# Kernel optimization log

Hardware: AMD Instinct MI355X
Metric: run time of the kernel (lower is better)

Reference implementation:

```python
import jax, jax.numpy as jnp
import numpy as np

N_NODES = 100000
N_EDGES = 1000000
D_IN = 64
D_OUT = 64


def setup_inputs() -> dict:
    key = jax.random.key(0)
    k1, k2, k3, k4, k5 = jax.random.split(key, 5)
    x = jax.random.normal(k1, (N_NODES, D_IN), dtype=jnp.float32)
    W = jax.random.normal(k2, (D_OUT, D_IN), dtype=jnp.float32) / np.sqrt(D_IN)
    edge_weights = jax.random.uniform(k3, (N_EDGES,), dtype=jnp.float32)
    source = jax.random.randint(k4, (N_EDGES,), 0, N_NODES, dtype=jnp.int64 if jax.config.read('jax_enable_x64') else jnp.int32)
    target = jax.random.randint(k5, (N_EDGES,), 0, N_NODES, dtype=jnp.int64 if jax.config.read('jax_enable_x64') else jnp.int32)
    return {"x": x, "W": W, "edge_weights": edge_weights,
            "source": source, "target": target, "num_nodes": N_NODES}


def reference(x, W, edge_weights, source, target, num_nodes):
    # Linear (no bias): h = x @ W^T, shape (num_nodes, out)
    h = jnp.einsum('nd,od->no', x, W)
    # Gather messages per edge, scale by edge weights
    msg = h[source] * edge_weights[:, None]  # (num_edges, out)
    # Scatter-add by target node (sum aggregation)
    delta = jax.ops.segment_sum(msg, target, num_segments=num_nodes)
    return delta
```

## Files before the change

### kernel.cpp

```cpp
#include <hip/hip_runtime.h>


#define D     64
#define BKT   64
#define BSH   6
#define NBMAX 2048
#define CAP   1024

__global__ __launch_bounds__(256) void gcn_scatter_kernel(
    const float* __restrict__ x, const float* __restrict__ ew,
    const int* __restrict__ src, const int* __restrict__ tgt,
    float* __restrict__ s, int n_edges)
{
    int lane = threadIdx.x & 63;
    int e = blockIdx.x * 4 + (threadIdx.x >> 6);
    if (e >= n_edges) return;
    int sn = src[e];
    int tn = tgt[e];
    float w = ew[e];
    float v = x[(size_t)sn * D + lane] * w;
    atomicAdd(&s[(size_t)tn * D + lane], v);
}

__global__ __launch_bounds__(256) void gcn_gemm_kernel(
    const float* __restrict__ s, const float* __restrict__ W,
    float* __restrict__ out, int n_nodes)
{
    __shared__ float4 xs[64 * 17];
    const int tid  = threadIdx.x;
    const int lane = tid & 63;
    const int wid  = __builtin_amdgcn_readfirstlane(tid >> 6);
    const int row0 = blockIdx.x * 64;

    const float4* s4 = reinterpret_cast<const float4*>(s);
#pragma unroll
    for (int k = 0; k < 4; ++k) {
        int f  = tid + k * 256;
        int r  = f >> 4;
        int c4 = f & 15;
        float4 v = make_float4(0.f, 0.f, 0.f, 0.f);
        if (row0 + r < n_nodes)
            v = s4[(size_t)(row0 + r) * 16 + c4];
        xs[r * 17 + c4] = v;
    }
    __syncthreads();

    float acc[16];
#pragma unroll
    for (int j = 0; j < 16; ++j) acc[j] = 0.f;

    const int o0 = wid * 16;
    const float4* W4 = reinterpret_cast<const float4*>(W);
#pragma unroll
    for (int d4 = 0; d4 < 16; ++d4) {
        float4 xv = xs[lane * 17 + d4];
#pragma unroll
        for (int j = 0; j < 16; ++j) {
            float4 wv = W4[(size_t)(o0 + j) * 16 + d4];
            acc[j] += xv.x * wv.x + xv.y * wv.y + xv.z * wv.z + xv.w * wv.w;
        }
    }

    const int row = row0 + lane;
    if (row < n_nodes) {
        float4* out4 = reinterpret_cast<float4*>(out);
#pragma unroll
        for (int j4 = 0; j4 < 4; ++j4) {
            float4 v = make_float4(acc[j4 * 4 + 0], acc[j4 * 4 + 1],
                                   acc[j4 * 4 + 2], acc[j4 * 4 + 3]);
            out4[(size_t)row * 16 + wid * 4 + j4] = v;
        }
    }
}

__device__ __forceinline__ unsigned f2bf(float f) {
    unsigned u = __float_as_uint(f);
    return (u + 0x7FFFu + ((u >> 16) & 1u)) >> 16;
}

__global__ __launch_bounds__(256) void convert_bf16_kernel(
    const float* __restrict__ x, uint2* __restrict__ xb, int n4)
{
    const float4* x4 = reinterpret_cast<const float4*>(x);
    int i = blockIdx.x * 256 + threadIdx.x;
    const int stride = gridDim.x * 256;
    for (; i < n4; i += stride) {
        float4 v = x4[i];
        uint2 o;
        o.x = f2bf(v.x) | (f2bf(v.y) << 16);
        o.y = f2bf(v.z) | (f2bf(v.w) << 16);
        xb[i] = o;
    }
}

__global__ __launch_bounds__(256) void bucket_hist_kernel(
    const int* __restrict__ tgt, int* __restrict__ bcnt,
    int n_edges, int nb, int epb)
{
    __shared__ int h[NBMAX];
    const int tid = threadIdx.x;
    for (int i = tid; i < nb; i += 256) h[i] = 0;
    __syncthreads();
    const int e0 = blockIdx.x * epb;
    const int e1 = min(e0 + epb, n_edges);
    for (int e = e0 + tid; e < e1; e += 256)
        atomicAdd(&h[tgt[e] >> BSH], 1);
    __syncthreads();
    for (int b = tid; b < nb; b += 256) {
        int c = h[b];
        if (c) atomicAdd(&bcnt[b], c);
    }
}

__global__ __launch_bounds__(1024) void bucket_scan_kernel(
    const int* __restrict__ bcnt, int* __restrict__ bstarts,
    int* __restrict__ bcur, int nb)
{
    __shared__ int lds[1024];
    const int tid = threadIdx.x;
    const int i0 = 2 * tid, i1 = 2 * tid + 1;
    int v0 = (i0 < nb) ? bcnt[i0] : 0;
    int v1 = (i1 < nb) ? bcnt[i1] : 0;
    int tsum = v0 + v1;
    lds[tid] = tsum;
    __syncthreads();
    for (int off = 1; off < 1024; off <<= 1) {
        int a = (tid >= off) ? lds[tid - off] : 0;
        __syncthreads();
        lds[tid] += a;
        __syncthreads();
    }
    int pre = lds[tid] - tsum;
    if (i0 < nb) { bstarts[i0] = pre;      bcur[i0] = pre; }
    if (i1 < nb) { bstarts[i1] = pre + v0; bcur[i1] = pre + v0; }
}

__global__ __launch_bounds__(256) void bucket_scatter_kernel(
    const int* __restrict__ src, const int* __restrict__ tgt,
    const float* __restrict__ ew, int* __restrict__ bcur,
    int2* __restrict__ pairs, int n_edges, int nb, int epb)
{
    __shared__ int h[NBMAX];
    __shared__ int base[NBMAX];
    const int tid = threadIdx.x;
    for (int i = tid; i < nb; i += 256) h[i] = 0;
    __syncthreads();
    const int e0 = blockIdx.x * epb;
    const int e1 = min(e0 + epb, n_edges);

    for (int e = e0 + tid; e < e1; e += 256)
        atomicAdd(&h[tgt[e] >> BSH], 1);
    __syncthreads();

    for (int b = tid; b < nb; b += 256) {
        int c = h[b];
        base[b] = c ? atomicAdd(&bcur[b], c) : 0;
        h[b] = 0;
    }
    __syncthreads();

    for (int e = e0 + tid; e < e1; e += 256) {
        int t = tgt[e];
        int b = t >> BSH;
        int r = atomicAdd(&h[b], 1);
        pairs[base[b] + r] =
            make_int2(((t & (BKT - 1)) << 24) | src[e], __float_as_int(ew[e]));
    }
}

__global__ __launch_bounds__(512, 6) void bucket_sort_reduce_gemm_kernel(
    const uint2* __restrict__ xb, const float* __restrict__ W,
    const int* __restrict__ bstarts, const int2* __restrict__ pairs,
    float* __restrict__ out, int n_nodes, int n_edges, int nb)
{
    __shared__ float Wl[64 * 66];
    __shared__ int2  ep[CAP];
    __shared__ int   segIncl[BKT];
    __shared__ int   rankc[BKT];
    __shared__ float accRow[8][64];

    const int tid  = threadIdx.x;
    const int lane = tid & 63;
    const int wv   = tid >> 6;
    const int q4   = lane >> 4;
    const int m    = lane & 15;

    for (int i = tid; i < 64 * 64; i += 512)
        Wl[(i >> 6) * 66 + (i & 63)] = W[i];

    const int b   = blockIdx.x;
    const int beg = bstarts[b];
    const int end = (b + 1 < nb) ? bstarts[b + 1] : n_edges;

    float4 acc[8];
#pragma unroll
    for (int s = 0; s < 8; ++s) acc[s] = make_float4(0.f, 0.f, 0.f, 0.f);

    for (int cbeg = beg; cbeg < end; cbeg += CAP) {
        const int ccnt = min(CAP, end - cbeg);

        if (tid < BKT) segIncl[tid] = 0;
        __syncthreads();

        for (int i = tid; i < ccnt; i += 512) {
            unsigned px = (unsigned)pairs[cbeg + i].x;
            atomicAdd(&segIncl[px >> 24], 1);
        }
        __syncthreads();

        int myc = (tid < BKT) ? segIncl[tid] : 0;
        __syncthreads();
        for (int off = 1; off < BKT; off <<= 1) {
            int a = (tid < BKT && tid >= off) ? segIncl[tid - off] : 0;
            __syncthreads();
            if (tid < BKT) segIncl[tid] += a;
            __syncthreads();
        }
        if (tid < BKT) rankc[tid] = segIncl[tid] - myc;
        __syncthreads();

        for (int i = tid; i < ccnt; i += 512) {
            int2 p = pairs[cbeg + i];
            int tl = ((unsigned)p.x) >> 24;
            int pos = atomicAdd(&rankc[tl], 1);
            ep[pos] = p;
        }
        __syncthreads();

#pragma unroll
        for (int s = 0; s < 8; ++s) {
            const int tl = s * 8 + wv;
            const int s0 = __builtin_amdgcn_readfirstlane(tl ? segIncl[tl - 1] : 0);
            const int s1 = __builtin_amdgcn_readfirstlane(segIncl[tl]);
            float4 a = acc[s];
            for (int e = s0; e < s1; e += 8) {
                const int ea = e + q4;
                const int eb = e + 4 + q4;
                int2 p0 = ep[min(ea, s1 - 1)];
                int2 p1 = ep[min(eb, s1 - 1)];
                float w0 = (ea < s1) ? __int_as_float(p0.y) : 0.f;
                float w1 = (eb < s1) ? __int_as_float(p1.y) : 0.f;
                uint2 r0 = xb[(size_t)(p0.x & 0xFFFFFF) * 16 + m];
                uint2 r1 = xb[(size_t)(p1.x & 0xFFFFFF) * 16 + m];
                a.x += w0 * __uint_as_float(r0.x << 16);
                a.y += w0 * __uint_as_float(r0.x & 0xFFFF0000u);
                a.z += w0 * __uint_as_float(r0.y << 16);
                a.w += w0 * __uint_as_float(r0.y & 0xFFFF0000u);
                a.x += w1 * __uint_as_float(r1.x << 16);
                a.y += w1 * __uint_as_float(r1.x & 0xFFFF0000u);
                a.z += w1 * __uint_as_float(r1.y << 16);
                a.w += w1 * __uint_as_float(r1.y & 0xFFFF0000u);
            }
            acc[s] = a;
        }
        __syncthreads();
    }

    const int node0 = b * BKT;
#pragma unroll
    for (int s = 0; s < 8; ++s) {
        const int node = node0 + s * 8 + wv;
        if (node < n_nodes) {
            float4 a = acc[s];
            a.x += __shfl_xor(a.x, 16); a.y += __shfl_xor(a.y, 16);
            a.z += __shfl_xor(a.z, 16); a.w += __shfl_xor(a.w, 16);
            a.x += __shfl_xor(a.x, 32); a.y += __shfl_xor(a.y, 32);
            a.z += __shfl_xor(a.z, 32); a.w += __shfl_xor(a.w, 32);
            if (lane < 16)
                *reinterpret_cast<float4*>(&accRow[wv][m * 4]) = a;
            asm volatile("s_waitcnt lgkmcnt(0)" ::: "memory");

            float o = 0.f;
            const float2* a2 = reinterpret_cast<const float2*>(&accRow[wv][0]);
            const float2* w2 = reinterpret_cast<const float2*>(&Wl[lane * 66]);
#pragma unroll
            for (int d2 = 0; d2 < 32; ++d2) {
                float2 aq = a2[d2];
                float2 wq = w2[d2];
                o += aq.x * wq.x + aq.y * wq.y;
            }
            out[(size_t)node * D + lane] = o;
            asm volatile("s_waitcnt lgkmcnt(0)" ::: "memory");
        }
    }
}

extern "C" void kernel_launch(void* const* d_in, const int* in_sizes, int n_in,
                              void* d_out, int out_size, void* d_ws, size_t ws_size,
                              hipStream_t stream)
{
    const float* x   = (const float*)d_in[0];
    const float* W   = (const float*)d_in[1];
    const float* ew  = (const float*)d_in[2];
    const int*   src = (const int*)d_in[3];
    const int*   tgt = (const int*)d_in[4];

    const int n_nodes = in_sizes[0] / D;
    const int n_edges = in_sizes[2];
    const int nb = (n_nodes + BKT - 1) / BKT;

    int*  bcnt    = (int*)d_ws;
    int*  bstarts = bcnt + NBMAX;
    int*  bcur    = bstarts + NBMAX;
    int2* pairs   = (int2*)(bcur + NBMAX);
    uint2* xb     = (uint2*)(pairs + n_edges);

    const size_t need = (size_t)3 * NBMAX * sizeof(int) +
                        (size_t)n_edges * sizeof(int2) +
                        (size_t)n_nodes * 16 * sizeof(uint2);

    if (nb > NBMAX || n_nodes > (1 << 24) || ws_size < need) {
        float* s = (float*)d_ws;
        hipMemsetAsync(s, 0, (size_t)n_nodes * D * sizeof(float), stream);
        gcn_scatter_kernel<<<(n_edges + 3) / 4, 256, 0, stream>>>(x, ew, src, tgt, s, n_edges);
        gcn_gemm_kernel<<<(n_nodes + 63) / 64, 256, 0, stream>>>(s, W, (float*)d_out, n_nodes);
        return;
    }

    hipMemsetAsync(bcnt, 0, (size_t)nb * sizeof(int), stream);

    convert_bf16_kernel<<<1024, 256, 0, stream>>>(x, xb, n_nodes * 16);

    const int ablocks = 256;
    const int epbA = (n_edges + ablocks - 1) / ablocks;
    bucket_hist_kernel<<<ablocks, 256, 0, stream>>>(tgt, bcnt, n_edges, nb, epbA);

    bucket_scan_kernel<<<1, 1024, 0, stream>>>(bcnt, bstarts, bcur, nb);

    const int cblocks = 256;
    const int epbC = (n_edges + cblocks - 1) / cblocks;
    bucket_scatter_kernel<<<cblocks, 256, 0, stream>>>(src, tgt, ew, bcur,
                                                       pairs, n_edges, nb, epbC);

    bucket_sort_reduce_gemm_kernel<<<nb, 512, 0, stream>>>(
        xb, W, bstarts, pairs, (float*)d_out, n_nodes, n_edges, nb);
}
```

Measured before the change: 128.0 us.

## Fuse bf16 conversion with histogram, register-cache W rows, wave-shuffle scan

Merges the bf16 conversion of x and the target-bucket histogram into one kernel, which removes a launch. In the final kernel, the 64x64 W tile is no longer staged in LDS. Each lane instead loads its W row into 16 float4 registers after the aggregation loop, and the GEMV reads accRow as float4. The multi-barrier LDS prefix scan over 64 segments becomes a single-wave __shfl_up scan, and the occupancy hint drops from 6 to 4. The trade-off is higher register pressure, and the conversion now runs on only 256 blocks instead of 1024.

```diff
diff --git a/kernel.cpp b/kernel.cpp
--- a/kernel.cpp
+++ b/kernel.cpp
@@ -78,29 +78,25 @@
     return (u + 0x7FFFu + ((u >> 16) & 1u)) >> 16;
 }
 
-__global__ __launch_bounds__(256) void convert_bf16_kernel(
-    const float* __restrict__ x, uint2* __restrict__ xb, int n4)
-{
+__global__ __launch_bounds__(256) void convert_hist_kernel(
+    const float* __restrict__ x, uint2* __restrict__ xb, int n4,
+    const int* __restrict__ tgt, int* __restrict__ bcnt,
+    int n_edges, int nb, int epb)
+{
+    __shared__ int h[NBMAX];
+    const int tid = threadIdx.x;
+    for (int i = tid; i < nb; i += 256) h[i] = 0;
+
     const float4* x4 = reinterpret_cast<const float4*>(x);
-    int i = blockIdx.x * 256 + threadIdx.x;
-    const int stride = gridDim.x * 256;
-    for (; i < n4; i += stride) {
+    for (int i = blockIdx.x * 256 + tid; i < n4; i += gridDim.x * 256) {
         float4 v = x4[i];
         uint2 o;
         o.x = f2bf(v.x) | (f2bf(v.y) << 16);
         o.y = f2bf(v.z) | (f2bf(v.w) << 16);
         xb[i] = o;
     }
-}
-
-__global__ __launch_bounds__(256) void bucket_hist_kernel(
-    const int* __restrict__ tgt, int* __restrict__ bcnt,
-    int n_edges, int nb, int epb)
-{
-    __shared__ int h[NBMAX];
-    const int tid = threadIdx.x;
-    for (int i = tid; i < nb; i += 256) h[i] = 0;
-    __syncthreads();
+    __syncthreads();
+
     const int e0 = blockIdx.x * epb;
     const int e1 = min(e0 + epb, n_edges);
     for (int e = e0 + tid; e < e1; e += 256)
@@ -168,16 +164,15 @@
     }
 }
 
-__global__ __launch_bounds__(512, 6) void bucket_sort_reduce_gemm_kernel(
+__global__ __launch_bounds__(512, 4) void bucket_sort_reduce_gemm_kernel(
     const uint2* __restrict__ xb, const float* __restrict__ W,
     const int* __restrict__ bstarts, const int2* __restrict__ pairs,
     float* __restrict__ out, int n_nodes, int n_edges, int nb)
 {
-    __shared__ float Wl[64 * 66];
     __shared__ int2  ep[CAP];
     __shared__ int   segIncl[BKT];
     __shared__ int   rankc[BKT];
-    __shared__ float accRow[8][64];
+    __shared__ __align__(16) float accRow[8][64];
 
     const int tid  = threadIdx.x;
     const int lane = tid & 63;
@@ -185,9 +180,6 @@
     const int q4   = lane >> 4;
     const int m    = lane & 15;
 
-    for (int i = tid; i < 64 * 64; i += 512)
-        Wl[(i >> 6) * 66 + (i & 63)] = W[i];
-
     const int b   = blockIdx.x;
     const int beg = bstarts[b];
     const int end = (b + 1 < nb) ? bstarts[b + 1] : n_edges;
@@ -208,15 +200,17 @@
         }
         __syncthreads();
 
-        int myc = (tid < BKT) ? segIncl[tid] : 0;
-        __syncthreads();
-        for (int off = 1; off < BKT; off <<= 1) {
-            int a = (tid < BKT && tid >= off) ? segIncl[tid - off] : 0;
-            __syncthreads();
-            if (tid < BKT) segIncl[tid] += a;
-            __syncthreads();
-        }
-        if (tid < BKT) rankc[tid] = segIncl[tid] - myc;
+        if (wv == 0) {
+            int c0 = segIncl[lane];
+            int v = c0;
+#pragma unroll
+            for (int off = 1; off < 64; off <<= 1) {
+                int n = __shfl_up(v, off);
+                if (lane >= off) v += n;
+            }
+            segIncl[lane] = v;
+            rankc[lane]   = v - c0;
+        }
         __syncthreads();
 
         for (int i = tid; i < ccnt; i += 512) {
@@ -256,6 +250,13 @@
         __syncthreads();
     }
 
+    float4 wr4[16];
+    {
+        const float4* Wrow = reinterpret_cast<const float4*>(W + lane * D);
+#pragma unroll
+        for (int i = 0; i < 16; ++i) wr4[i] = Wrow[i];
+    }
+
     const int node0 = b * BKT;
 #pragma unroll
     for (int s = 0; s < 8; ++s) {
@@ -271,13 +272,12 @@
             asm volatile("s_waitcnt lgkmcnt(0)" ::: "memory");
 
             float o = 0.f;
-            const float2* a2 = reinterpret_cast<const float2*>(&accRow[wv][0]);
-            const float2* w2 = reinterpret_cast<const float2*>(&Wl[lane * 66]);
-#pragma unroll
-            for (int d2 = 0; d2 < 32; ++d2) {
-                float2 aq = a2[d2];
-                float2 wq = w2[d2];
-                o += aq.x * wq.x + aq.y * wq.y;
+            const float4* a4p = reinterpret_cast<const float4*>(&accRow[wv][0]);
+#pragma unroll
+            for (int d4 = 0; d4 < 16; ++d4) {
+                float4 aq = a4p[d4];
+                float4 wq = wr4[d4];
+                o += aq.x * wq.x + aq.y * wq.y + aq.z * wq.z + aq.w * wq.w;
             }
             out[(size_t)node * D + lane] = o;
             asm volatile("s_waitcnt lgkmcnt(0)" ::: "memory");
@@ -319,11 +319,10 @@
 
     hipMemsetAsync(bcnt, 0, (size_t)nb * sizeof(int), stream);
 
-    convert_bf16_kernel<<<1024, 256, 0, stream>>>(x, xb, n_nodes * 16);
-
     const int ablocks = 256;
     const int epbA = (n_edges + ablocks - 1) / ablocks;
-    bucket_hist_kernel<<<ablocks, 256, 0, stream>>>(tgt, bcnt, n_edges, nb, epbA);
+    convert_hist_kernel<<<ablocks, 256, 0, stream>>>(x, xb, n_nodes * 16,
+                                                     tgt, bcnt, n_edges, nb, epbA);
 
     bucket_scan_kernel<<<1, 1024, 0, stream>>>(bcnt, bstarts, bcur, nb);
 
```

Measured after the change: 135.3 us. 1.06x slower.
